# Kernel optimization log

Measured on AMD Instinct MI355X. Metric: run time of the kernel, lower is better.

## Reference

```python
import jax, jax.numpy as jnp
import numpy as np

EPS = 1e-5


def setup_inputs() -> dict:
    key = jax.random.key(0)
    k1, k2, k3 = jax.random.split(key, 3)
    B, n_per, C_in, C_out = 8, 131072, 32, 64
    N = B * n_per
    coord = jax.random.uniform(k1, (N, 3), dtype=jnp.float32)          # points in unit cube
    feat = jax.random.normal(k2, (N, C_in), dtype=jnp.float32)
    offset = (jnp.arange(1, B + 1, dtype=jnp.int32) * n_per)           # cumulative counts
    W = jax.random.normal(k3, (C_in, C_out), dtype=jnp.float32) * 0.05  # fc weight (no bias)
    gamma = jnp.ones((C_out,), dtype=jnp.float32)
    beta = jnp.zeros((C_out,), dtype=jnp.float32)
    return {"coord": coord, "feat": feat, "offset": offset, "W": W,
            "gamma": gamma, "beta": beta, "grid_size": 0.05}


def reference(coord, feat, offset, W, gamma, beta, grid_size):
    N = coord.shape[0]
    B = offset.shape[0]
    # offset2batch: point i belongs to batch = first b with i < offset[b]
    batch = jnp.searchsorted(offset, jnp.arange(N, dtype=offset.dtype), side="right").astype(jnp.int32)

    # fc -> BatchNorm (training-mode batch stats, biased var) -> ReLU
    h = feat @ W                                                        # [N, C_out]
    mean = h.mean(axis=0)
    var = jnp.mean((h - mean) ** 2, axis=0)
    h = jax.nn.relu((h - mean) * jax.lax.rsqrt(var + EPS) * gamma + beta)

    # start = per-batch min coord (segment_csr 'min' over batch pointer)
    start = jax.ops.segment_min(coord, batch, num_segments=B)           # [B, 3]

    # voxel_grid: integer voxel coords per point, combined with batch into a unique key
    v = jnp.floor((coord - start[batch]) / grid_size).astype(jnp.int32)  # [N, 3] >= 0
    D = v.max(axis=0) + 1                                               # grid extents
    vkey = ((batch * D[0] + v[:, 0]) * D[1] + v[:, 1]) * D[2] + v[:, 2]

    # unique(sorted) + inverse + counts; then segment mean/max by cluster
    uniq, inverse, counts = jnp.unique(vkey, return_inverse=True, return_counts=True)
    inverse = inverse.reshape(-1).astype(jnp.int32)
    M = uniq.shape[0]
    coord_out = jax.ops.segment_sum(coord, inverse, num_segments=M) / counts[:, None].astype(coord.dtype)
    feat_out = jax.ops.segment_max(h, inverse, num_segments=M)

    # batch id of each cluster (constant within cluster) -> new offset
    batch_out = jax.ops.segment_min(batch, inverse, num_segments=M)
    offset_out = jnp.cumsum(jnp.bincount(batch_out, length=B)).astype(offset.dtype)
    return coord_out, feat_out, offset_out, inverse
```

## Files before the change

kernel.cpp:

```cpp
#include <hip/hip_runtime.h>
#include <float.h>

#define EPSV 1e-5f
#define DGRID 21
#define DPROD (21 * 21 * 21)

typedef __attribute__((ext_vector_type(8))) short bf16x8;
typedef __attribute__((ext_vector_type(4))) float f32x4;

__device__ __forceinline__ short f2bf(float x) {
    unsigned u = __float_as_uint(x);
    unsigned r = (u + 0x7FFFu + ((u >> 16) & 1u)) >> 16;
    return (short)r;
}

__device__ __forceinline__ int batch_of(int i, const int* __restrict__ offset, int B) {
    int b = 0;
    while (b < B - 1 && i >= offset[b]) ++b;
    return b;
}

__global__ void k_init(int* startEnc, int B) {
    int tid = threadIdx.x;
    if (tid < B * 3) startEnc[tid] = 0x7FFFFFFF;
}

__global__ void k_start(const float* __restrict__ coord, const int* __restrict__ offset,
                        int* startEnc, int* counts, int KSM, int N, int B) {
    int gtid = blockIdx.x * blockDim.x + threadIdx.x;
    for (int k = gtid; k < KSM; k += gridDim.x * blockDim.x) counts[k] = 0;

    __shared__ int smin[24];
    int t = threadIdx.x;
    if (t < B * 3) smin[t] = 0x7FFFFFFF;
    __syncthreads();
    int base = gtid * 4;
    int curb = -1;
    int m0 = 0x7FFFFFFF, m1 = 0x7FFFFFFF, m2 = 0x7FFFFFFF;
    for (int r = 0; r < 4; ++r) {
        int i = base + r;
        if (i >= N) break;
        int b = batch_of(i, offset, B);
        if (b != curb) {
            if (curb >= 0) {
                atomicMin(&smin[curb * 3 + 0], m0);
                atomicMin(&smin[curb * 3 + 1], m1);
                atomicMin(&smin[curb * 3 + 2], m2);
            }
            curb = b; m0 = m1 = m2 = 0x7FFFFFFF;
        }
        m0 = min(m0, __float_as_int(coord[(size_t)i * 3 + 0]));
        m1 = min(m1, __float_as_int(coord[(size_t)i * 3 + 1]));
        m2 = min(m2, __float_as_int(coord[(size_t)i * 3 + 2]));
    }
    if (curb >= 0) {
        atomicMin(&smin[curb * 3 + 0], m0);
        atomicMin(&smin[curb * 3 + 1], m1);
        atomicMin(&smin[curb * 3 + 2], m2);
    }
    __syncthreads();
    if (t < B * 3 && smin[t] != 0x7FFFFFFF) atomicMin(&startEnc[t], smin[t]);
}

__global__ void k_count(const float* __restrict__ coord, const int* __restrict__ offset,
                        const int* __restrict__ startEnc, const float* __restrict__ gsP,
                        int* counts, int2* __restrict__ vr, int N, int B) {
    int i = blockIdx.x * blockDim.x + threadIdx.x;
    if (i >= N) return;
    float inv_gs = 1.0f / gsP[0];
    int b = batch_of(i, offset, B);
    float s0 = __int_as_float(startEnc[b * 3 + 0]);
    float s1 = __int_as_float(startEnc[b * 3 + 1]);
    float s2 = __int_as_float(startEnc[b * 3 + 2]);
    int vx = min(DGRID - 1, (int)floorf((coord[(size_t)i * 3 + 0] - s0) * inv_gs));
    int vy = min(DGRID - 1, (int)floorf((coord[(size_t)i * 3 + 1] - s1) * inv_gs));
    int vz = min(DGRID - 1, (int)floorf((coord[(size_t)i * 3 + 2] - s2) * inv_gs));
    int k = ((b * DGRID + vx) * DGRID + vy) * DGRID + vz;
    int r = atomicAdd(&counts[k], 1);
    vr[i] = make_int2(k, r);
}

__global__ void k_scan1(const int* __restrict__ counts, int* occPart, int* cntPart, int KSM) {
    __shared__ int so[256], sc[256];
    int t = threadIdx.x;
    int base = blockIdx.x * 1024 + t * 4;
    int o = 0, c = 0;
    for (int r = 0; r < 4; ++r) {
        int k = base + r;
        if (k < KSM) { int cnt = counts[k]; o += (cnt > 0); c += cnt; }
    }
    so[t] = o; sc[t] = c;
    __syncthreads();
    for (int s = 128; s > 0; s >>= 1) {
        if (t < s) { so[t] += so[t + s]; sc[t] += sc[t + s]; }
        __syncthreads();
    }
    if (t == 0) { occPart[blockIdx.x] = so[0]; cntPart[blockIdx.x] = sc[0]; }
}

__global__ void k_scan3(const int* __restrict__ counts,
                        const int* __restrict__ occPart, const int* __restrict__ cntPart,
                        int2* krec, int* cntC, int* cstartC, int KSM, int NBLK) {
    __shared__ int so[256], sc[256];
    __shared__ int po[128], pc[128];
    __shared__ int poEx, pcEx;
    int t = threadIdx.x;

    if (t < 128) {
        po[t] = (t < NBLK) ? occPart[t] : 0;
        pc[t] = (t < NBLK) ? cntPart[t] : 0;
    }
    __syncthreads();
    for (int s = 1; s < 128; s <<= 1) {
        int ao = 0, ac = 0;
        if (t < 128 && t >= s) { ao = po[t - s]; ac = pc[t - s]; }
        __syncthreads();
        if (t < 128) { po[t] += ao; pc[t] += ac; }
        __syncthreads();
    }
    if (t == 0) {
        int b = blockIdx.x;
        poEx = (b == 0) ? 0 : po[b - 1];
        pcEx = (b == 0) ? 0 : pc[b - 1];
    }
    __syncthreads();

    int base = blockIdx.x * 1024 + t * 4;
    int o[4], c[4];
    int tO = 0, tC = 0;
    for (int r = 0; r < 4; ++r) {
        int k = base + r;
        int cnt = (k < KSM) ? counts[k] : 0;
        o[r] = (cnt > 0); c[r] = cnt;
        tO += o[r]; tC += c[r];
    }
    so[t] = tO; sc[t] = tC;
    __syncthreads();
    for (int s = 1; s < 256; s <<= 1) {
        int ao = 0, ac = 0;
        if (t >= s) { ao = so[t - s]; ac = sc[t - s]; }
        __syncthreads();
        so[t] += ao; sc[t] += ac;
        __syncthreads();
    }
    int exO = so[t] - tO + poEx;
    int exC = sc[t] - tC + pcEx;
    for (int r = 0; r < 4; ++r) {
        int k = base + r;
        if (k < KSM) {
            krec[k] = make_int2(exO, exC);
            if (c[r] > 0) { cntC[exO] = c[r]; cstartC[exO] = exC; }
            exO += o[r]; exC += c[r];
        }
    }
}

__global__ void k_pos(const int2* __restrict__ vr, const int2* __restrict__ krec,
                      int* __restrict__ plist, float* __restrict__ dout,
                      int N, int B, int M) {
    int i = blockIdx.x * blockDim.x + threadIdx.x;
    if (i >= N) return;
    int2 v = vr[i];
    int2 rec = krec[v.x];
    plist[rec.y + v.y] = i;
    dout[(size_t)67 * M + B + i] = (float)rec.x;
}

__global__ void k_mat(const int* __restrict__ plist,
                      const float* __restrict__ feat, const float* __restrict__ coord,
                      short* __restrict__ featR, float* __restrict__ coordR, int N) {
    int pos = blockIdx.x * blockDim.x + threadIdx.x;
    if (pos >= N) return;
    int i = plist[pos];
    const float4* fp = reinterpret_cast<const float4*>(feat + (size_t)i * 32);
    bf16x8* dst = reinterpret_cast<bf16x8*>(featR + (size_t)pos * 32);
#pragma unroll
    for (int t = 0; t < 4; ++t) {
        float4 a = fp[2 * t];
        float4 b2 = fp[2 * t + 1];
        bf16x8 r;
        r[0] = f2bf(a.x);  r[1] = f2bf(a.y);  r[2] = f2bf(a.z);  r[3] = f2bf(a.w);
        r[4] = f2bf(b2.x); r[5] = f2bf(b2.y); r[6] = f2bf(b2.z); r[7] = f2bf(b2.w);
        dst[t] = r;
    }
    float4 cv;
    cv.x = coord[(size_t)i * 3 + 0];
    cv.y = coord[(size_t)i * 3 + 1];
    cv.z = coord[(size_t)i * 3 + 2];
    cv.w = 0.f;
    *reinterpret_cast<float4*>(coordR + (size_t)pos * 4) = cv;
}

__launch_bounds__(64)
__global__ void k_pool(const short* __restrict__ featR, const float* __restrict__ coordR,
                       const float* __restrict__ W,
                       const int* __restrict__ cstartC, const int* __restrict__ cntC,
                       float* __restrict__ dout, float* __restrict__ statPart, int M) {
    const int lane = threadIdx.x;
    const int col  = lane & 15;
    const int quad = lane >> 4;
    const int nw = gridDim.x;
    const int gw = blockIdx.x;

    bf16x8 Bf[4];
#pragma unroll
    for (int t = 0; t < 4; ++t) {
#pragma unroll
        for (int j = 0; j < 8; ++j) {
            int k = quad * 8 + j;
            Bf[t][j] = f2bf(W[k * 64 + t * 16 + col]);
        }
    }

    float sumA[4] = {0.f, 0.f, 0.f, 0.f};
    float sqA[4]  = {0.f, 0.f, 0.f, 0.f};

    for (int c0 = 2 * gw; c0 < M; c0 += 2 * nw) {
        int c1 = c0 + 1;
        bool has2 = (c1 < M);
        if (!has2) c1 = c0;
        int ps0 = cstartC[c0], n0 = cntC[c0];
        int ps1 = cstartC[c1], n1 = cntC[c1];
        int nmax = max(n0, n1);

        float maxA0[4] = {-FLT_MAX, -FLT_MAX, -FLT_MAX, -FLT_MAX};
        float maxA1[4] = {-FLT_MAX, -FLT_MAX, -FLT_MAX, -FLT_MAX};
        float cacc0 = 0.f, cacc1 = 0.f;

        for (int base = 0; base < nmax; base += 16) {
            int m = base + col;
            int idx0 = min(m, n0 - 1);
            int idx1 = min(m, n1 - 1);
            bf16x8 Af0 = *reinterpret_cast<const bf16x8*>(featR + (size_t)(ps0 + idx0) * 32 + quad * 8);
            bf16x8 Af1 = *reinterpret_cast<const bf16x8*>(featR + (size_t)(ps1 + idx1) * 32 + quad * 8);
            if (quad > 0) {
                float v0 = coordR[(size_t)(ps0 + idx0) * 4 + (quad - 1)];
                float v1 = coordR[(size_t)(ps1 + idx1) * 4 + (quad - 1)];
                cacc0 += (m < n0) ? v0 : 0.f;
                cacc1 += (m < n1) ? v1 : 0.f;
            }
            f32x4 Cz = {0.f, 0.f, 0.f, 0.f};
#pragma unroll
            for (int t = 0; t < 4; ++t) {
                f32x4 v0 = __builtin_amdgcn_mfma_f32_16x16x32_bf16(Af0, Bf[t], Cz, 0, 0, 0);
                f32x4 v1 = __builtin_amdgcn_mfma_f32_16x16x32_bf16(Af1, Bf[t], Cz, 0, 0, 0);
#pragma unroll
                for (int r = 0; r < 4; ++r) {
                    int rowPt = base + quad * 4 + r;
                    maxA0[t] = fmaxf(maxA0[t], v0[r]);
                    maxA1[t] = fmaxf(maxA1[t], v1[r]);
                    float m0 = (rowPt < n0) ? v0[r] : 0.f;
                    sumA[t] += m0; sqA[t] = fmaf(m0, m0, sqA[t]);
                    float m1 = (rowPt < n1 && has2) ? v1[r] : 0.f;
                    sumA[t] += m1; sqA[t] = fmaf(m1, m1, sqA[t]);
                }
            }
        }
        float out0 = 0.f, out1 = 0.f;
#pragma unroll
        for (int t = 0; t < 4; ++t) {
            float v = maxA0[t];
            v = fmaxf(v, __shfl_xor(v, 16, 64));
            v = fmaxf(v, __shfl_xor(v, 32, 64));
            if (quad == t) out0 = v;
            float w = maxA1[t];
            w = fmaxf(w, __shfl_xor(w, 16, 64));
            w = fmaxf(w, __shfl_xor(w, 32, 64));
            if (quad == t) out1 = w;
        }
        dout[(size_t)3 * M + (size_t)c0 * 64 + lane] = out0;
        dout[(size_t)3 * M + (size_t)c1 * 64 + lane] = out1;

        cacc0 += __shfl_xor(cacc0, 1, 64); cacc0 += __shfl_xor(cacc0, 2, 64);
        cacc0 += __shfl_xor(cacc0, 4, 64); cacc0 += __shfl_xor(cacc0, 8, 64);
        cacc1 += __shfl_xor(cacc1, 1, 64); cacc1 += __shfl_xor(cacc1, 2, 64);
        cacc1 += __shfl_xor(cacc1, 4, 64); cacc1 += __shfl_xor(cacc1, 8, 64);
        if (quad > 0 && col == 0) {
            dout[(size_t)c0 * 3 + (quad - 1)] = cacc0 / (float)n0;
            dout[(size_t)c1 * 3 + (quad - 1)] = cacc1 / (float)n1;
        }
    }

    float so = 0.f, qo = 0.f;
#pragma unroll
    for (int t = 0; t < 4; ++t) {
        float s = sumA[t];
        s += __shfl_xor(s, 16, 64);
        s += __shfl_xor(s, 32, 64);
        float q = sqA[t];
        q += __shfl_xor(q, 16, 64);
        q += __shfl_xor(q, 32, 64);
        if (quad == t) { so = s; qo = q; }
    }
    statPart[(size_t)gw * 128 + lane] = so;
    statPart[(size_t)gw * 128 + 64 + lane] = qo;
}

__global__ void k_statred(const float* __restrict__ statPart,
                          const float* __restrict__ gamma, const float* __restrict__ beta,
                          float* bnA, float* bnB, int NB, int N) {
    __shared__ float s1[256], s2[256];
    int c = blockIdx.x;
    int t = threadIdx.x;
    float a = 0.f, b = 0.f;
    for (int bb = t; bb < NB; bb += 256) {
        a += statPart[(size_t)bb * 128 + c];
        b += statPart[(size_t)bb * 128 + 64 + c];
    }
    s1[t] = a; s2[t] = b;
    __syncthreads();
    for (int s = 128; s > 0; s >>= 1) {
        if (t < s) { s1[t] += s1[t + s]; s2[t] += s2[t + s]; }
        __syncthreads();
    }
    if (t == 0) {
        float invN = 1.0f / (float)N;
        float mean = s1[0] * invN;
        float var = s2[0] * invN - mean * mean;
        float aa = gamma[c] / sqrtf(var + EPSV);
        bnA[c] = aa;
        bnB[c] = beta[c] - mean * aa;
    }
}

__global__ void k_final(float* __restrict__ dout, const float* __restrict__ bnA,
                        const float* __restrict__ bnB,
                        const int2* __restrict__ krec, int M, int B) {
    size_t stride = (size_t)gridDim.x * blockDim.x;
    size_t tid0 = (size_t)blockIdx.x * blockDim.x + threadIdx.x;
    size_t totF = (size_t)M * 64;
    for (size_t t = tid0; t < totF; t += stride) {
        int c = (int)(t & 63);
        float v = dout[(size_t)3 * M + t];
        dout[(size_t)3 * M + t] = fmaxf(bnA[c] * v + bnB[c], 0.f);
    }
    if (tid0 < (size_t)B) {
        int val = (tid0 == (size_t)(B - 1)) ? M : krec[(size_t)(tid0 + 1) * DPROD].x;
        dout[(size_t)67 * M + tid0] = (float)val;
    }
}

extern "C" void kernel_launch(void* const* d_in, const int* in_sizes, int n_in,
                              void* d_out, int out_size, void* d_ws, size_t ws_size,
                              hipStream_t stream) {
    const float* coord = (const float*)d_in[0];
    const float* feat  = (const float*)d_in[1];
    const int*   offset = (const int*)d_in[2];
    const float* W     = (const float*)d_in[3];
    const float* gamma = (const float*)d_in[4];
    const float* beta  = (const float*)d_in[5];
    const float* gsP   = (const float*)d_in[6];
    float* dout = (float*)d_out;

    const int N = in_sizes[0] / 3;
    const int B = in_sizes[2];
    const int M = (out_size - B - N) / 67;
    const int KSM = B * DPROD;
    const int NBLK = (KSM + 1023) / 1024;
    const int NBPL = 8192;

    int* wsI = (int*)d_ws;
    int* startEnc  = wsI + 0;
    float* bnA     = (float*)(wsI + 64);
    float* bnB     = (float*)(wsI + 128);
    int* occPart   = wsI + 256;
    int* cntPart   = wsI + 384;
    int* counts    = wsI + 1024;
    int2* krec     = (int2*)(counts + KSM);
    int* cntC      = (int*)(krec + KSM);
    int* cstartC   = cntC + KSM;
    int2* vr       = (int2*)(cstartC + KSM);
    int* plist     = (int*)(vr + N);
    float* statPart = (float*)(plist + N);
    short* featR   = (short*)(statPart + (size_t)NBPL * 128);
    float* coordR  = (float*)(featR + (size_t)N * 32);

    const int TPB = 256;
    int gChunk = (N + 1023) / 1024;
    int gPoint = (N + TPB - 1) / TPB;

    k_init<<<1, 64, 0, stream>>>(startEnc, B);
    k_start<<<gChunk, TPB, 0, stream>>>(coord, offset, startEnc, counts, KSM, N, B);
    k_count<<<gPoint, TPB, 0, stream>>>(coord, offset, startEnc, gsP, counts, vr, N, B);
    k_scan1<<<NBLK, TPB, 0, stream>>>(counts, occPart, cntPart, KSM);
    k_scan3<<<NBLK, TPB, 0, stream>>>(counts, occPart, cntPart, krec, cntC, cstartC, KSM, NBLK);
    k_pos<<<gPoint, TPB, 0, stream>>>(vr, krec, plist, dout, N, B, M);
    k_mat<<<gPoint, TPB, 0, stream>>>(plist, feat, coord, featR, coordR, N);
    k_pool<<<NBPL, 64, 0, stream>>>(featR, coordR, W, cstartC, cntC, dout, statPart, M);
    k_statred<<<64, 256, 0, stream>>>(statPart, gamma, beta, bnA, bnB, NBPL, N);
    k_final<<<1024, TPB, 0, stream>>>(dout, bnA, bnB, krec, M, B);
}
```

Measured before the change: 380.9 us.

## Fuse gather and bf16 conversion into pooling kernel, drop reordered copies

Removes the k_mat pass that wrote cluster-ordered bf16 features and padded coords. k_pool now reads the point index from plist and gathers fp32 features and coords straight from the original arrays, converting to bf16 in registers. This saves one full write and re-read of the feature data, but turns the pool loads into scattered 128-byte row reads and adds an extra indirection. The cluster pairing also changes from adjacent clusters (c0, c0+1) to clusters nw apart.

```diff
diff --git a/kernel.cpp b/kernel.cpp
--- a/kernel.cpp
+++ b/kernel.cpp
@@ -166,35 +166,11 @@
     dout[(size_t)67 * M + B + i] = (float)rec.x;
 }
 
-__global__ void k_mat(const int* __restrict__ plist,
-                      const float* __restrict__ feat, const float* __restrict__ coord,
-                      short* __restrict__ featR, float* __restrict__ coordR, int N) {
-    int pos = blockIdx.x * blockDim.x + threadIdx.x;
-    if (pos >= N) return;
-    int i = plist[pos];
-    const float4* fp = reinterpret_cast<const float4*>(feat + (size_t)i * 32);
-    bf16x8* dst = reinterpret_cast<bf16x8*>(featR + (size_t)pos * 32);
-#pragma unroll
-    for (int t = 0; t < 4; ++t) {
-        float4 a = fp[2 * t];
-        float4 b2 = fp[2 * t + 1];
-        bf16x8 r;
-        r[0] = f2bf(a.x);  r[1] = f2bf(a.y);  r[2] = f2bf(a.z);  r[3] = f2bf(a.w);
-        r[4] = f2bf(b2.x); r[5] = f2bf(b2.y); r[6] = f2bf(b2.z); r[7] = f2bf(b2.w);
-        dst[t] = r;
-    }
-    float4 cv;
-    cv.x = coord[(size_t)i * 3 + 0];
-    cv.y = coord[(size_t)i * 3 + 1];
-    cv.z = coord[(size_t)i * 3 + 2];
-    cv.w = 0.f;
-    *reinterpret_cast<float4*>(coordR + (size_t)pos * 4) = cv;
-}
-
 __launch_bounds__(64)
-__global__ void k_pool(const short* __restrict__ featR, const float* __restrict__ coordR,
+__global__ void k_pool(const float* __restrict__ feat, const float* __restrict__ coord,
                        const float* __restrict__ W,
                        const int* __restrict__ cstartC, const int* __restrict__ cntC,
+                       const int* __restrict__ plist,
                        float* __restrict__ dout, float* __restrict__ statPart, int M) {
     const int lane = threadIdx.x;
     const int col  = lane & 15;
@@ -215,9 +191,9 @@
     float sumA[4] = {0.f, 0.f, 0.f, 0.f};
     float sqA[4]  = {0.f, 0.f, 0.f, 0.f};
 
-    for (int c0 = 2 * gw; c0 < M; c0 += 2 * nw) {
-        int c1 = c0 + 1;
-        bool has2 = (c1 < M);
+    for (int c0 = gw; c0 < M; c0 += 2 * nw) {
+        int c1 = c0 + nw;
+        bool has2 = c1 < M;
         if (!has2) c1 = c0;
         int ps0 = cstartC[c0], n0 = cntC[c0];
         int ps1 = cstartC[c1], n1 = cntC[c1];
@@ -231,14 +207,23 @@
             int m = base + col;
             int idx0 = min(m, n0 - 1);
             int idx1 = min(m, n1 - 1);
-            bf16x8 Af0 = *reinterpret_cast<const bf16x8*>(featR + (size_t)(ps0 + idx0) * 32 + quad * 8);
-            bf16x8 Af1 = *reinterpret_cast<const bf16x8*>(featR + (size_t)(ps1 + idx1) * 32 + quad * 8);
+            int p0 = plist[ps0 + idx0];
+            int p1 = plist[ps1 + idx1];
+            const float4* r0p = reinterpret_cast<const float4*>(feat + (size_t)p0 * 32 + quad * 8);
+            const float4* r1p = reinterpret_cast<const float4*>(feat + (size_t)p1 * 32 + quad * 8);
+            float4 a00 = r0p[0], a01 = r0p[1];
+            float4 a10 = r1p[0], a11 = r1p[1];
             if (quad > 0) {
-                float v0 = coordR[(size_t)(ps0 + idx0) * 4 + (quad - 1)];
-                float v1 = coordR[(size_t)(ps1 + idx1) * 4 + (quad - 1)];
+                float v0 = coord[(size_t)p0 * 3 + (quad - 1)];
+                float v1 = coord[(size_t)p1 * 3 + (quad - 1)];
                 cacc0 += (m < n0) ? v0 : 0.f;
                 cacc1 += (m < n1) ? v1 : 0.f;
             }
+            bf16x8 Af0, Af1;
+            Af0[0] = f2bf(a00.x); Af0[1] = f2bf(a00.y); Af0[2] = f2bf(a00.z); Af0[3] = f2bf(a00.w);
+            Af0[4] = f2bf(a01.x); Af0[5] = f2bf(a01.y); Af0[6] = f2bf(a01.z); Af0[7] = f2bf(a01.w);
+            Af1[0] = f2bf(a10.x); Af1[1] = f2bf(a10.y); Af1[2] = f2bf(a10.z); Af1[3] = f2bf(a10.w);
+            Af1[4] = f2bf(a11.x); Af1[5] = f2bf(a11.y); Af1[6] = f2bf(a11.z); Af1[7] = f2bf(a11.w);
             f32x4 Cz = {0.f, 0.f, 0.f, 0.f};
 #pragma unroll
             for (int t = 0; t < 4; ++t) {
@@ -372,8 +357,6 @@
     int2* vr       = (int2*)(cstartC + KSM);
     int* plist     = (int*)(vr + N);
     float* statPart = (float*)(plist + N);
-    short* featR   = (short*)(statPart + (size_t)NBPL * 128);
-    float* coordR  = (float*)(featR + (size_t)N * 32);
 
     const int TPB = 256;
     int gChunk = (N + 1023) / 1024;
@@ -385,8 +368,7 @@
     k_scan1<<<NBLK, TPB, 0, stream>>>(counts, occPart, cntPart, KSM);
     k_scan3<<<NBLK, TPB, 0, stream>>>(counts, occPart, cntPart, krec, cntC, cstartC, KSM, NBLK);
     k_pos<<<gPoint, TPB, 0, stream>>>(vr, krec, plist, dout, N, B, M);
-    k_mat<<<gPoint, TPB, 0, stream>>>(plist, feat, coord, featR, coordR, N);
-    k_pool<<<NBPL, 64, 0, stream>>>(featR, coordR, W, cstartC, cntC, dout, statPart, M);
+    k_pool<<<NBPL, 64, 0, stream>>>(feat, coord, W, cstartC, cntC, plist, dout, statPart, M);
     k_statred<<<64, 256, 0, stream>>>(statPart, gamma, beta, bnA, bnB, NBPL, N);
     k_final<<<1024, TPB, 0, stream>>>(dout, bnA, bnB, krec, M, B);
 }
```

Measured after the change: 348.2 us. 1.09x faster.
